# Kernel tuning notes

Measured on AMD Instinct MI355X. Metric: run time of the kernel, lower is better.

The kernel has to match this reference:

```python
import jax, jax.numpy as jnp
import numpy as np

N, E = 50000, 800000
IN_C, OUT_C, D_EMB = 64, 64, 64
NEG_SLOPE = 0.2  # GDN GraphLayer default leaky_relu slope


def setup_inputs() -> dict:
    key = jax.random.key(0)
    ks = jax.random.split(key, 9)
    return {
        "x": jax.random.normal(ks[0], (N, IN_C), jnp.float32),
        "edge_index": jax.random.randint(ks[1], (2, E), 0, N, dtype=jnp.int32),
        "embedding": jax.random.normal(ks[2], (N, D_EMB), jnp.float32),
        # learned params of GraphLayer (heads=1, concat)
        "W": jax.random.normal(ks[3], (OUT_C, IN_C), jnp.float32) * (1.0 / np.sqrt(IN_C)),
        "att_i": jax.random.normal(ks[4], (OUT_C,), jnp.float32) * 0.1,
        "att_j": jax.random.normal(ks[5], (OUT_C,), jnp.float32) * 0.1,
        "att_em_i": jax.random.normal(ks[6], (D_EMB,), jnp.float32) * 0.1,
        "att_em_j": jax.random.normal(ks[7], (D_EMB,), jnp.float32) * 0.1,
        "bias": jax.random.normal(ks[8], (OUT_C,), jnp.float32) * 0.01,
    }


def reference(x, edge_index, embedding, W, att_i, att_j, att_em_i, att_em_j, bias):
    n = x.shape[0]
    loops = jnp.arange(n, dtype=edge_index.dtype)
    src = jnp.concatenate([edge_index[0], loops])  # message source j
    dst = jnp.concatenate([edge_index[1], loops])  # message target i

    h = x @ W.T  # [N, OUT_C]
    # per-node attention scores (equivalent to cat(h, emb) . cat(att, att_em))
    s_i = h @ att_i + embedding @ att_em_i  # [N]
    s_j = h @ att_j + embedding @ att_em_j  # [N]

    alpha = s_i[dst] + s_j[src]                         # [E+N] edge logits
    alpha = jax.nn.leaky_relu(alpha, NEG_SLOPE)
    # softmax over incoming edges of each destination node
    amax = jax.ops.segment_max(alpha, dst, num_segments=n)
    ex = jnp.exp(alpha - amax[dst])
    denom = jax.ops.segment_sum(ex, dst, num_segments=n)
    alpha = ex / (denom[dst] + 1e-16)

    msg = h[src] * alpha[:, None]                       # [E+N, OUT_C]
    out = jax.ops.segment_sum(msg, dst, num_segments=n) + bias
    return jax.nn.relu(out)
```

## Files before the change

### kernel.cpp

```cpp
#include <hip/hip_runtime.h>
#include <hip/hip_bf16.h>
#include <math.h>

#define NEG_SLOPE 0.2f

#define XTA(k, r) ((k) * 64 + ((r) ^ ((((k) >> 2) & 7) << 2)))

__device__ __forceinline__ void gemm_tile(
    float* lds, int t, int tid,
    const float* __restrict__ x, const float* __restrict__ emb,
    const float* __restrict__ W,
    const float* __restrict__ att_i, const float* __restrict__ att_j,
    const float* __restrict__ att_em_i, const float* __restrict__ att_em_j,
    __hip_bfloat16* __restrict__ h, float* __restrict__ s_i,
    float* __restrict__ s_j, int N)
{
    float* XT = lds;
    float* WT = lds + 4096;

    const int rbase = t * 64;
    const int valid = min(64, N - rbase);

    #pragma unroll
    for (int i = 0; i < 4; ++i) {
        int idx = i * 256 + tid;
        int r = idx >> 4, m = idx & 15;
        float4 v = make_float4(0.f, 0.f, 0.f, 0.f);
        if (r < valid)
            v = *reinterpret_cast<const float4*>(x + (size_t)(rbase + r) * 64 + 4 * m);
        int k = 4 * m;
        XT[XTA(k + 0, r)] = v.x;
        XT[XTA(k + 1, r)] = v.y;
        XT[XTA(k + 2, r)] = v.z;
        XT[XTA(k + 3, r)] = v.w;
    }
    #pragma unroll
    for (int i = 0; i < 4; ++i) {
        int idx = i * 256 + tid;
        int c = idx >> 4, m = idx & 15;
        float4 v = *reinterpret_cast<const float4*>(W + idx * 4);
        int k = 4 * m;
        WT[XTA(k + 0, c)] = v.x;
        WT[XTA(k + 1, c)] = v.y;
        WT[XTA(k + 2, c)] = v.z;
        WT[XTA(k + 3, c)] = v.w;
    }
    __syncthreads();

    const int cg_ = tid & 15, rg = tid >> 4;
    const int c0 = cg_ * 4, r0 = rg * 4;
    float acc[4][4];
    #pragma unroll
    for (int a = 0; a < 4; ++a)
        #pragma unroll
        for (int q = 0; q < 4; ++q) acc[a][q] = 0.f;

    #pragma unroll 4
    for (int k = 0; k < 64; ++k) {
        float4 wv = *reinterpret_cast<float4*>(&WT[XTA(k, c0)]);
        float4 xa = *reinterpret_cast<float4*>(&XT[XTA(k, r0)]);
        float xs[4] = {xa.x, xa.y, xa.z, xa.w};
        float ws[4] = {wv.x, wv.y, wv.z, wv.w};
        #pragma unroll
        for (int a = 0; a < 4; ++a)
            #pragma unroll
            for (int q = 0; q < 4; ++q)
                acc[a][q] = fmaf(ws[a], xs[q], acc[a][q]);
    }

    #pragma unroll
    for (int q = 0; q < 4; ++q) {
        int r = r0 + q;
        if (r < valid) {
            union { __hip_bfloat16 p[4]; uint2 u; } pk;
            pk.p[0] = __float2bfloat16(acc[0][q]);
            pk.p[1] = __float2bfloat16(acc[1][q]);
            pk.p[2] = __float2bfloat16(acc[2][q]);
            pk.p[3] = __float2bfloat16(acc[3][q]);
            *reinterpret_cast<uint2*>(h + (size_t)(rbase + r) * 64 + c0) = pk.u;
        }
    }

    float ai[4], aj[4];
    #pragma unroll
    for (int a = 0; a < 4; ++a) { ai[a] = att_i[c0 + a]; aj[a] = att_j[c0 + a]; }

    __syncthreads();
    float* RED_I = lds;
    float* RED_J = lds + 1088;
    float* EMT   = lds + 4096;

    #pragma unroll
    for (int q = 0; q < 4; ++q) {
        int r = r0 + q;
        float pi = acc[0][q]*ai[0] + acc[1][q]*ai[1] + acc[2][q]*ai[2] + acc[3][q]*ai[3];
        float pj = acc[0][q]*aj[0] + acc[1][q]*aj[1] + acc[2][q]*aj[2] + acc[3][q]*aj[3];
        RED_I[r * 17 + cg_] = pi;
        RED_J[r * 17 + cg_] = pj;
    }
    #pragma unroll
    for (int i = 0; i < 4; ++i) {
        int idx = i * 256 + tid;
        int r = idx >> 4, m = idx & 15;
        float4 v = make_float4(0.f, 0.f, 0.f, 0.f);
        if (r < valid)
            v = *reinterpret_cast<const float4*>(emb + (size_t)(rbase + r) * 64 + 4 * m);
        int k = 4 * m;
        EMT[XTA(k + 0, r)] = v.x;
        EMT[XTA(k + 1, r)] = v.y;
        EMT[XTA(k + 2, r)] = v.z;
        EMT[XTA(k + 3, r)] = v.w;
    }
    __syncthreads();

    if (tid < 64 && tid < valid) {
        float ri = 0.f, rj = 0.f;
        #pragma unroll
        for (int j = 0; j < 16; ++j) {
            ri += RED_I[tid * 17 + j];
            rj += RED_J[tid * 17 + j];
        }
        float ei = 0.f, ej = 0.f;
        #pragma unroll 16
        for (int k = 0; k < 64; ++k) {
            float ev = EMT[XTA(k, tid)];
            ei = fmaf(ev, att_em_i[k], ei);
            ej = fmaf(ev, att_em_j[k], ej);
        }
        s_i[rbase + tid] = ri + ei;
        s_j[rbase + tid] = rj + ej;
    }
}

__global__ __launch_bounds__(256) void k_gemm_scatter(
    const float* __restrict__ x, const float* __restrict__ emb,
    const float* __restrict__ W,
    const float* __restrict__ att_i, const float* __restrict__ att_j,
    const float* __restrict__ att_em_i, const float* __restrict__ att_em_j,
    const int* __restrict__ srcA, const int* __restrict__ dstA,
    int* __restrict__ cursor, unsigned short* __restrict__ csr,
    __hip_bfloat16* __restrict__ h, float* __restrict__ s_i,
    float* __restrict__ s_j, int N, int E, int GB, int sh, int nchunks)
{
    __shared__ float lds[8192];
    const int tid = threadIdx.x;

    if ((int)blockIdx.x >= GB) {
        const int b2    = blockIdx.x - GB;
        const int oct   = b2 & 7;
        const int chunk = b2 >> 3;
        const int npos  = nchunks * 256;
        const int E4    = E >> 2;
        const int4* d4p = reinterpret_cast<const int4*>(dstA);
        const int4* s4p = reinterpret_cast<const int4*>(srcA);
        for (int p = chunk * 256 + tid; p < E4; p += npos) {
            int4 d4 = d4p[p];
            bool m0 = (d4.x >> sh) == oct, m1 = (d4.y >> sh) == oct;
            bool m2 = (d4.z >> sh) == oct, m3 = (d4.w >> sh) == oct;
            if (m0 | m1 | m2 | m3) {
                int4 s4 = s4p[p];
                if (m0) { int pos = atomicAdd(&cursor[d4.x], 1);
                          if (pos < 64) csr[(size_t)d4.x * 64 + pos] = (unsigned short)s4.x; }
                if (m1) { int pos = atomicAdd(&cursor[d4.y], 1);
                          if (pos < 64) csr[(size_t)d4.y * 64 + pos] = (unsigned short)s4.y; }
                if (m2) { int pos = atomicAdd(&cursor[d4.z], 1);
                          if (pos < 64) csr[(size_t)d4.z * 64 + pos] = (unsigned short)s4.z; }
                if (m3) { int pos = atomicAdd(&cursor[d4.w], 1);
                          if (pos < 64) csr[(size_t)d4.w * 64 + pos] = (unsigned short)s4.w; }
            }
        }
        for (int e = E4 * 4 + chunk * 256 + tid; e < E; e += npos) {
            int d = dstA[e];
            if ((d >> sh) == oct) {
                int pos = atomicAdd(&cursor[d], 1);
                if (pos < 64)
                    csr[(size_t)d * 64 + pos] = (unsigned short)srcA[e];
            }
        }
        return;
    }

    gemm_tile(lds, blockIdx.x, tid, x, emb, W, att_i, att_j,
              att_em_i, att_em_j, h, s_i, s_j, N);
}

__global__ __launch_bounds__(256) void k_aggregate(
    const __hip_bfloat16* __restrict__ h, const float* __restrict__ s_i,
    const float* __restrict__ s_j, const int* __restrict__ cursor,
    const unsigned short* __restrict__ csr, const float* __restrict__ bias,
    float* __restrict__ out, int N)
{
    __shared__ uint2 tbl[4][64];
    const int tid  = threadIdx.x;
    const int lane = tid & 63;
    const int wid  = tid >> 6;
    const int node = (blockIdx.x * blockDim.x + tid) >> 6;
    if (node >= N) return;

    int deg_e = cursor[node];
    deg_e = (deg_e > 63) ? 63 : deg_e;
    const int degT = deg_e + 1;
    const float si = s_i[node];

    int s = node;
    if (lane < deg_e) s = csr[(size_t)node * 64 + lane];
    float ex = 0.f;
    if (lane < degT) {
        float a = si + s_j[s];
        a = (a > 0.f) ? a : NEG_SLOPE * a;
        ex = __expf(a);
    }
    float l = ex;
    #pragma unroll
    for (int off = 32; off > 0; off >>= 1) l += __shfl_xor(l, off);

    tbl[wid][lane] = make_uint2(__float_as_uint(ex), (unsigned)s);

    const int q  = lane >> 4;
    const int c4 = lane & 15;
    const uint2* hp2 = reinterpret_cast<const uint2*>(h);
    float a0 = 0.f, a1 = 0.f, a2 = 0.f, a3 = 0.f;

    const int iters = (degT + 3) >> 2;
    #pragma unroll 2
    for (int it = 0; it < iters; ++it) {
        uint2 rec = tbl[wid][4 * it + q];
        float e = __uint_as_float(rec.x);
        int   t = (int)rec.y;
        uint2 u = hp2[(size_t)t * 16 + c4];
        a0 = fmaf(e, __uint_as_float(u.x << 16), a0);
        a1 = fmaf(e, __uint_as_float(u.x & 0xffff0000u), a1);
        a2 = fmaf(e, __uint_as_float(u.y << 16), a2);
        a3 = fmaf(e, __uint_as_float(u.y & 0xffff0000u), a3);
    }

    a0 += __shfl_xor(a0, 16); a0 += __shfl_xor(a0, 32);
    a1 += __shfl_xor(a1, 16); a1 += __shfl_xor(a1, 32);
    a2 += __shfl_xor(a2, 16); a2 += __shfl_xor(a2, 32);
    a3 += __shfl_xor(a3, 16); a3 += __shfl_xor(a3, 32);

    if (lane < 16) {
        float inv = 1.f / (l + 1e-16f);
        float4 bv = *reinterpret_cast<const float4*>(bias + 4 * c4);
        float4 o;
        o.x = fmaxf(a0 * inv + bv.x, 0.f);
        o.y = fmaxf(a1 * inv + bv.y, 0.f);
        o.z = fmaxf(a2 * inv + bv.z, 0.f);
        o.w = fmaxf(a3 * inv + bv.w, 0.f);
        *reinterpret_cast<float4*>(out + (size_t)node * 64 + 4 * c4) = o;
    }
}

extern "C" void kernel_launch(void* const* d_in, const int* in_sizes, int n_in,
                              void* d_out, int out_size, void* d_ws, size_t ws_size,
                              hipStream_t stream) {
    const float* x        = (const float*)d_in[0];
    const int*   ei       = (const int*)  d_in[1];
    const float* emb      = (const float*)d_in[2];
    const float* W        = (const float*)d_in[3];
    const float* att_i    = (const float*)d_in[4];
    const float* att_j    = (const float*)d_in[5];
    const float* att_em_i = (const float*)d_in[6];
    const float* att_em_j = (const float*)d_in[7];
    const float* bias     = (const float*)d_in[8];
    float* out = (float*)d_out;

    const int N = in_sizes[0] / 64;
    const int E = in_sizes[1] / 2;
    const int* e_src = ei;
    const int* e_dst = ei + E;

    char* ws = (char*)d_ws;
    __hip_bfloat16* h = (__hip_bfloat16*)ws;  ws += (size_t)N * 64 * 2;
    float* s_i     = (float*)ws;  ws += (size_t)N * 4;
    float* s_j     = (float*)ws;  ws += (size_t)N * 4;
    int*   cursor  = (int*)ws;    ws += (size_t)N * 4;
    unsigned short* csr = (unsigned short*)ws;  ws += (size_t)N * 64 * 2;

    int sh = 0;
    while ((1 << sh) < N) ++sh;
    sh -= 3;

    const int GB = (N + 63) / 64;
    const int NCHUNK = 256;

    hipMemsetAsync(cursor, 0, (size_t)N * 4, stream);
    k_gemm_scatter<<<GB + NCHUNK * 8, 256, 0, stream>>>(
        x, emb, W, att_i, att_j, att_em_i, att_em_j,
        e_src, e_dst, cursor, csr, h, s_i, s_j, N, E, GB, sh, NCHUNK);
    k_aggregate<<<(N * 64 + 255) / 256, 256, 0, stream>>>(h, s_i, s_j, cursor,
                                                          csr, bias, out, N);
}
```

Measured before the change: 153.4 us.

## Replace per-node global atomic CSR scatter with two-level bucketed binning and placement

The edge scatter becomes a two-pass bucket sort. First, edges are binned into 64 destination buckets, using LDS-local lists that are flushed to per-bucket global FIFOs with one atomic per bucket per block. A new k_place kernel then builds each bucket's CSR rows and degree counts with LDS atomics. This removes per-edge global atomics on per-node cursors and the 8x redundant dst reads across octants. The cost is an extra kernel launch, FIFO traffic, and only 64 blocks in k_place, which limits parallelism, plus fixed capacity caps that could drop edges under skew.

```diff
diff --git a/kernel.cpp b/kernel.cpp
--- a/kernel.cpp
+++ b/kernel.cpp
@@ -5,6 +5,11 @@
 #define NEG_SLOPE 0.2f
 
 #define XTA(k, r) ((k) * 64 + ((r) ^ ((((k) >> 2) & 7) << 2)))
+
+#define NBUK 64
+#define SCAT 512
+#define LCAP 120
+#define FCAP 20480
 
 __device__ __forceinline__ void gemm_tile(
     float* lds, int t, int tid,
@@ -138,43 +143,61 @@
     const float* __restrict__ att_i, const float* __restrict__ att_j,
     const float* __restrict__ att_em_i, const float* __restrict__ att_em_j,
     const int* __restrict__ srcA, const int* __restrict__ dstA,
-    int* __restrict__ cursor, unsigned short* __restrict__ csr,
+    int* __restrict__ fcur, unsigned* __restrict__ fifo,
     __hip_bfloat16* __restrict__ h, float* __restrict__ s_i,
-    float* __restrict__ s_j, int N, int E, int GB, int sh, int nchunks)
+    float* __restrict__ s_j, int N, int E, int GB, int sh)
 {
     __shared__ float lds[8192];
     const int tid = threadIdx.x;
 
     if ((int)blockIdx.x >= GB) {
-        const int b2    = blockIdx.x - GB;
-        const int oct   = b2 & 7;
-        const int chunk = b2 >> 3;
-        const int npos  = nchunks * 256;
-        const int E4    = E >> 2;
+        const int b2 = blockIdx.x - GB;
+        int*      lcnt = reinterpret_cast<int*>(lds);
+        unsigned* lst  = reinterpret_cast<unsigned*>(lcnt + NBUK);
+        for (int i = tid; i < NBUK; i += 256) lcnt[i] = 0;
+        __syncthreads();
+
+        const int npos = SCAT * 256;
+        const int E4 = E >> 2;
         const int4* d4p = reinterpret_cast<const int4*>(dstA);
         const int4* s4p = reinterpret_cast<const int4*>(srcA);
-        for (int p = chunk * 256 + tid; p < E4; p += npos) {
+        const unsigned ml = (1u << sh) - 1u;
+
+        #define PUT(dd, ss) do {                                             \
+            int _b = (int)((unsigned)(dd) >> sh);                            \
+            unsigned _w = ((unsigned)(ss) << 16) | ((unsigned)(dd) & ml);    \
+            int _lp = atomicAdd(&lcnt[_b], 1);                               \
+            if (_lp < LCAP) lst[_b * LCAP + _lp] = _w;                       \
+            else { int _gp = atomicAdd(&fcur[_b], 1);                        \
+                   if (_gp < FCAP) fifo[(size_t)_b * FCAP + _gp] = _w; }     \
+        } while (0)
+
+        for (int p = b2 * 256 + tid; p < E4; p += npos) {
             int4 d4 = d4p[p];
-            bool m0 = (d4.x >> sh) == oct, m1 = (d4.y >> sh) == oct;
-            bool m2 = (d4.z >> sh) == oct, m3 = (d4.w >> sh) == oct;
-            if (m0 | m1 | m2 | m3) {
-                int4 s4 = s4p[p];
-                if (m0) { int pos = atomicAdd(&cursor[d4.x], 1);
-                          if (pos < 64) csr[(size_t)d4.x * 64 + pos] = (unsigned short)s4.x; }
-                if (m1) { int pos = atomicAdd(&cursor[d4.y], 1);
-                          if (pos < 64) csr[(size_t)d4.y * 64 + pos] = (unsigned short)s4.y; }
-                if (m2) { int pos = atomicAdd(&cursor[d4.z], 1);
-                          if (pos < 64) csr[(size_t)d4.z * 64 + pos] = (unsigned short)s4.z; }
-                if (m3) { int pos = atomicAdd(&cursor[d4.w], 1);
-                          if (pos < 64) csr[(size_t)d4.w * 64 + pos] = (unsigned short)s4.w; }
-            }
-        }
-        for (int e = E4 * 4 + chunk * 256 + tid; e < E; e += npos) {
-            int d = dstA[e];
-            if ((d >> sh) == oct) {
-                int pos = atomicAdd(&cursor[d], 1);
-                if (pos < 64)
-                    csr[(size_t)d * 64 + pos] = (unsigned short)srcA[e];
+            int4 s4 = s4p[p];
+            PUT(d4.x, s4.x);
+            PUT(d4.y, s4.y);
+            PUT(d4.z, s4.z);
+            PUT(d4.w, s4.w);
+        }
+        for (int e = E4 * 4 + b2 * 256 + tid; e < E; e += npos) {
+            int dd = dstA[e], ss = srcA[e];
+            PUT(dd, ss);
+        }
+        #undef PUT
+        __syncthreads();
+
+        const int lane = tid & 63, wid = tid >> 6;
+        for (int b = wid; b < NBUK; b += 4) {
+            int cnt = lcnt[b];
+            if (cnt > LCAP) cnt = LCAP;
+            int base = 0;
+            if (lane == 0 && cnt > 0) base = atomicAdd(&fcur[b], cnt);
+            base = __shfl(base, 0);
+            for (int i = lane; i < cnt; i += 64) {
+                int gp = base + i;
+                if (gp < FCAP)
+                    fifo[(size_t)b * FCAP + gp] = lst[b * LCAP + i];
             }
         }
         return;
@@ -182,6 +205,39 @@
 
     gemm_tile(lds, blockIdx.x, tid, x, emb, W, att_i, att_j,
               att_em_i, att_em_j, h, s_i, s_j, N);
+}
+
+__global__ __launch_bounds__(256) void k_place(
+    const unsigned* __restrict__ fifo, const int* __restrict__ fcur,
+    unsigned short* __restrict__ csr, int* __restrict__ cursor,
+    int N, int sh)
+{
+    __shared__ int lcnt[2048];
+    const int tid = threadIdx.x;
+    const int b = blockIdx.x;
+    const int range = 1 << sh;
+    const int base = b << sh;
+
+    for (int i = tid; i < range; i += 256) lcnt[i] = 0;
+    __syncthreads();
+
+    int cnt = fcur[b];
+    if (cnt > FCAP) cnt = FCAP;
+    const unsigned* f = fifo + (size_t)b * FCAP;
+    for (int i = tid; i < cnt; i += 256) {
+        unsigned w = f[i];
+        int dloc = (int)(w & (unsigned)(range - 1));
+        int s = (int)(w >> 16);
+        int pos = atomicAdd(&lcnt[dloc], 1);
+        if (pos < 64)
+            csr[(size_t)(base + dloc) * 64 + pos] = (unsigned short)s;
+    }
+    __syncthreads();
+
+    for (int i = tid; i < range; i += 256) {
+        int node = base + i;
+        if (node < N) cursor[node] = lcnt[i];
+    }
 }
 
 __global__ __launch_bounds__(256) void k_aggregate(
@@ -276,18 +332,19 @@
     float* s_j     = (float*)ws;  ws += (size_t)N * 4;
     int*   cursor  = (int*)ws;    ws += (size_t)N * 4;
     unsigned short* csr = (unsigned short*)ws;  ws += (size_t)N * 64 * 2;
+    unsigned* fifo = (unsigned*)ws;  ws += (size_t)NBUK * FCAP * 4;
+    int*   fcur    = (int*)ws;    ws += NBUK * 4;
 
     int sh = 0;
-    while ((1 << sh) < N) ++sh;
-    sh -= 3;
+    while (((N - 1) >> sh) >= NBUK) ++sh;
 
     const int GB = (N + 63) / 64;
-    const int NCHUNK = 256;
-
-    hipMemsetAsync(cursor, 0, (size_t)N * 4, stream);
-    k_gemm_scatter<<<GB + NCHUNK * 8, 256, 0, stream>>>(
+
+    hipMemsetAsync(fcur, 0, NBUK * sizeof(int), stream);
+    k_gemm_scatter<<<GB + SCAT, 256, 0, stream>>>(
         x, emb, W, att_i, att_j, att_em_i, att_em_j,
-        e_src, e_dst, cursor, csr, h, s_i, s_j, N, E, GB, sh, NCHUNK);
+        e_src, e_dst, fcur, fifo, h, s_i, s_j, N, E, GB, sh);
+    k_place<<<NBUK, 256, 0, stream>>>(fifo, fcur, csr, cursor, N, sh);
     k_aggregate<<<(N * 64 + 255) / 256, 256, 0, stream>>>(h, s_i, s_j, cursor,
                                                           csr, bias, out, N);
 }
```

Measured after the change: 317.2 us. +106.8%, slower.
